# Optimization experiments

Hardware: AMD Instinct MI355X
Metric: run time of the kernel (lower is better)

Reference implementation:

```python
import jax, jax.numpy as jnp
import numpy as np
import math

HQ, HKV, DH, WIN = 16, 4, 128, 512
RMS_EPS = 1.1920929e-07  # torch F.rms_norm default eps = fp32 machine eps


def _apply_rope(x, cos, sin):
    # x: [B,H,T,Dh]; interleaved-pair rotation as in the torch code
    x_even = x[..., ::2]
    x_odd = x[..., 1::2]
    x_rot = jnp.stack((-x_odd, x_even), axis=-1).reshape(x.shape)
    return x * cos + x_rot * sin


def _rms_norm(x):
    return x * jax.lax.rsqrt(jnp.mean(x * x, axis=-1, keepdims=True) + RMS_EPS)


def setup_inputs() -> dict:
    key = jax.random.key(0)
    k1, k2, k3 = jax.random.split(key, 3)
    B, T, C = 2, 2048, 2048
    x = jax.random.normal(k1, (B, T, C), dtype=jnp.float32)
    w_qkv = jax.random.normal(k2, ((HQ + 2 * HKV) * DH, C), dtype=jnp.float32) * 0.02
    w_proj = jax.random.normal(k3, (C, C), dtype=jnp.float32) * 0.02
    return {"x": x, "w_qkv": w_qkv, "w_proj": w_proj}


def reference(x, w_qkv, w_proj):
    B, T, C = x.shape
    rep = HQ // HKV
    qkv = x @ w_qkv.T  # [B,T,(Hq+2Hkv)*Dh]
    q, k, v = jnp.split(qkv, [HQ * DH, (HQ + HKV) * DH], axis=-1)
    Q = q.reshape(B, T, HQ, DH).transpose(0, 2, 1, 3)   # [B,Hq,T,Dh]
    K = k.reshape(B, T, HKV, DH).transpose(0, 2, 1, 3)  # [B,Hkv,T,Dh]
    V = v.reshape(B, T, HKV, DH).transpose(0, 2, 1, 3)
    # GQA expansion (repeat_interleave on head dim)
    K = jnp.repeat(K, rep, axis=1)
    V = jnp.repeat(V, rep, axis=1)
    # RoPE tables: freqs [T, Dh/2] -> cos/sin [1,1,T,Dh] via repeat_interleave(2)
    inv_freq = 1.0 / (10000.0 ** (jnp.arange(0, DH, 2, dtype=jnp.float32) / DH))
    freqs = jnp.arange(T, dtype=jnp.float32)[:, None] * inv_freq[None, :]
    cos = jnp.repeat(jnp.cos(freqs), 2, axis=-1)[None, None]
    sin = jnp.repeat(jnp.sin(freqs), 2, axis=-1)[None, None]
    Q = _rms_norm(_apply_rope(Q, cos, sin))
    K = _rms_norm(_apply_rope(K, cos, sin))
    scores = jnp.einsum('bhqd,bhkd->bhqk', Q, K) / math.sqrt(DH)
    i = jnp.arange(T)[:, None]
    j = jnp.arange(T)[None, :]
    mask = (i >= j) & ((i - j) < WIN)  # causal sliding window
    scores = jnp.where(mask[None, None], scores, -jnp.inf)
    attn = jax.nn.softmax(scores, axis=-1)
    y = jnp.einsum('bhqk,bhkd->bhqd', attn, V)
    y = y.transpose(0, 2, 1, 3).reshape(B, T, C)
    return y @ w_proj.T
```

## Files before the change

### kernel.cpp

```cpp
#include <hip/hip_runtime.h>
#include <stdint.h>

#define T_SEQ 2048
#define NB    2
#define DHD   128
#define NHQ   16
#define NHKV  4
#define SWIN  512
#define CDIM  2048
#define QKVN  3072
#define GBK   32

typedef __attribute__((ext_vector_type(8))) short short8;
typedef __attribute__((ext_vector_type(4))) float f32x4;
typedef __attribute__((ext_vector_type(16))) float f32x16;
typedef __attribute__((ext_vector_type(4))) unsigned int u32x4;
typedef __attribute__((address_space(3))) unsigned int lds_u32;
typedef __attribute__((address_space(1))) const unsigned int gbl_u32;

__device__ __forceinline__ unsigned short f2bf(float f) {
  unsigned int u = __float_as_uint(f);
  u += 0x7fffu + ((u >> 16) & 1u);
  return (unsigned short)(u >> 16);
}
__device__ __forceinline__ float bf2f(unsigned int h) {
  return __uint_as_float(h << 16);
}
__device__ __forceinline__ float exp2_fast(float x) {
  float r;
  asm("v_exp_f32 %0, %1" : "=v"(r) : "v"(x));
  return r;
}

__global__ __launch_bounds__(256) void k_f2bf3(const float* __restrict__ a, unsigned short* __restrict__ oa, int na4,
                                               const float* __restrict__ b, unsigned short* __restrict__ ob, int nb4,
                                               const float* __restrict__ c, unsigned short* __restrict__ oc, int nc4) {
  const int n = na4 + nb4 + nc4;
  for (int i = blockIdx.x * 256 + threadIdx.x; i < n; i += gridDim.x * 256) {
    const float* src; unsigned short* dst; int j = i;
    if (j < na4) { src = a; dst = oa; }
    else if (j < na4 + nb4) { j -= na4; src = b; dst = ob; }
    else { j -= na4 + nb4; src = c; dst = oc; }
    float4 v = reinterpret_cast<const float4*>(src)[j];
    uint2 o;
    o.x = ((unsigned int)f2bf(v.y) << 16) | f2bf(v.x);
    o.y = ((unsigned int)f2bf(v.w) << 16) | f2bf(v.z);
    reinterpret_cast<uint2*>(dst)[j] = o;
  }
}

__global__ __launch_bounds__(256) void k_trig(float* __restrict__ tbl) {
  int i = blockIdx.x * 256 + threadIdx.x;
  if (i >= T_SEQ * 64) return;
  int t = i >> 6, f = i & 63;
  float invf = powf(10000.f, -(float)f * (1.f / 64.f));
  float ang = (float)t * invf;
  tbl[i] = cosf(ang);
  tbl[T_SEQ * 64 + i] = sinf(ang);
}

template<int OUT_BF16>
__global__ __launch_bounds__(512) void k_gemm128(const unsigned short* __restrict__ A,
                                                 const unsigned short* __restrict__ B,
                                                 void* __restrict__ Cout,
                                                 int M, int N, int K, int nbx) {
  extern __shared__ __align__(16) char lds[];
  const int tid = threadIdx.x, lane = tid & 63, wid = tid >> 6;
  const int lr = lane & 15, lg = lane >> 4;
  const int wr = wid >> 2, wcn = wid & 3;

  const int nwg = gridDim.x, cpx = nwg >> 3;
  const int id = (int)blockIdx.x;
  const int sid = (id & 7) * cpx + (id >> 3);
  const int by = sid / nbx, bx = sid - by * nbx;

  const unsigned short* Ab = A + (size_t)by * 128 * K;
  const unsigned short* Bb = B + (size_t)bx * 256 * K;

  const int row0 = tid >> 2;
  const int blk  = tid & 3;
  const int col0 = ((blk * 16) ^ (((row0 >> 1) & 3) << 4)) >> 1;
  const unsigned short* pA0 = Ab + (size_t)row0 * K + col0;
  const unsigned short* pB0 = Bb + (size_t)row0 * K + col0;
  const unsigned short* pB1 = pB0 + (size_t)128 * K;

  const int sw  = ((lg ^ ((lr >> 1) & 3)) << 4);
  const int arb = (wr * 64 + lr) * 64 + sw;
  const int brb = (wcn * 64 + lr) * 64 + sw;

  f32x4 acc[4][4];
#pragma unroll
  for (int mi = 0; mi < 4; ++mi)
#pragma unroll
    for (int ni = 0; ni < 4; ++ni)
#pragma unroll
      for (int r = 0; r < 4; ++r) acc[mi][ni][r] = 0.f;

#define STAGE(t, sl_) do {                                                             \
    const int ko_ = (t) * GBK;                                                         \
    __builtin_amdgcn_global_load_lds((gbl_u32*)(pA0 + ko_),                            \
        (lds_u32*)(lds + (sl_) * 24576 + wid * 1024), 16, 0, 0);                       \
    __builtin_amdgcn_global_load_lds((gbl_u32*)(pB0 + ko_),                            \
        (lds_u32*)(lds + (sl_) * 24576 + 8192 + wid * 1024), 16, 0, 0);                \
    __builtin_amdgcn_global_load_lds((gbl_u32*)(pB1 + ko_),                            \
        (lds_u32*)(lds + (sl_) * 24576 + 16384 + wid * 1024), 16, 0, 0);               \
  } while (0)

#define COMPUTE(sl_) do {                                                              \
    const char* As_ = lds + (sl_) * 24576;                                             \
    const char* Bs_ = As_ + 8192;                                                      \
    short8 afr[4], bfr[4];                                                             \
    _Pragma("unroll") for (int mi = 0; mi < 4; ++mi)                                   \
      afr[mi] = *reinterpret_cast<const short8*>(As_ + arb + mi * 1024);               \
    _Pragma("unroll") for (int ni = 0; ni < 4; ++ni)                                   \
      bfr[ni] = *reinterpret_cast<const short8*>(Bs_ + brb + ni * 1024);               \
    __builtin_amdgcn_s_setprio(1);                                                     \
    _Pragma("unroll") for (int mi = 0; mi < 4; ++mi)                                   \
      _Pragma("unroll") for (int ni = 0; ni < 4; ++ni)                                 \
        acc[mi][ni] = __builtin_amdgcn_mfma_f32_16x16x32_bf16(afr[mi], bfr[ni],        \
                                                              acc[mi][ni], 0, 0, 0);   \
    __builtin_amdgcn_s_setprio(0);                                                     \
  } while (0)

#define WAITBAR(n) do {                                                                \
    asm volatile("s_waitcnt vmcnt(" #n ")" ::: "memory");                              \
    __builtin_amdgcn_s_barrier();                                                      \
    asm volatile("" ::: "memory");                                                     \
  } while (0)

  const int nt = K / GBK;
  STAGE(0, 0); STAGE(1, 1);
  int sc = 0, ss = 2;
  for (int t = 0; t < nt - 2; ++t) {
    WAITBAR(3);
    STAGE(t + 2, ss);
    COMPUTE(sc);
    sc = (sc == 2) ? 0 : sc + 1;
    ss = (ss == 2) ? 0 : ss + 1;
  }
  WAITBAR(3);
  COMPUTE(sc);
  sc = (sc == 2) ? 0 : sc + 1;
  WAITBAR(0);
  COMPUTE(sc);

#undef STAGE
#undef COMPUTE
#undef WAITBAR

#pragma unroll
  for (int mi = 0; mi < 4; ++mi) {
    const int row0c = by * 128 + wr * 64 + mi * 16 + lg * 4;
#pragma unroll
    for (int ni = 0; ni < 4; ++ni) {
      const int col = bx * 256 + wcn * 64 + ni * 16 + lr;
#pragma unroll
      for (int r = 0; r < 4; ++r) {
        size_t idx = (size_t)(row0c + r) * N + col;
        if (OUT_BF16) ((unsigned short*)Cout)[idx] = f2bf(acc[mi][ni][r]);
        else          ((float*)Cout)[idx] = acc[mi][ni][r];
      }
    }
  }
}

__global__ __launch_bounds__(256) void k_rope_rms(const unsigned short* __restrict__ qkv,
                                                  const float* __restrict__ tbl,
                                                  unsigned short* __restrict__ Qo,
                                                  unsigned short* __restrict__ Ko) {
  const int lane = threadIdx.x & 63, wid = threadIdx.x >> 6;
  const int job = blockIdx.x * 4 + wid;
  const int row = job / 20;
  const int hh  = job - row * 20;
  const int b = row >> 11, t = row & (T_SEQ - 1);
  const unsigned short* src;
  unsigned short* dst;
  float scale;
  if (hh < NHQ) {
    src = qkv + (size_t)row * QKVN + hh * DHD;
    dst = Qo + (((size_t)b * NHQ + hh) * T_SEQ + t) * DHD;
    scale = 0.1275173019f;
  } else {
    int h = hh - NHQ;
    src = qkv + (size_t)row * QKVN + CDIM + h * DHD;
    dst = Ko + (((size_t)b * NHKV + h) * T_SEQ + t) * DHD;
    scale = 1.f;
  }
  unsigned int pr = *reinterpret_cast<const unsigned int*>(src + lane * 2);
  float xe = bf2f(pr & 0xffffu), xo = bf2f(pr >> 16);
  float c = tbl[t * 64 + lane], s = tbl[T_SEQ * 64 + t * 64 + lane];
  float e = xe * c - xo * s;
  float o = xo * c + xe * s;
  float ss = e * e + o * o;
#pragma unroll
  for (int off = 1; off < 64; off <<= 1) ss += __shfl_xor(ss, off);
  float rn = rsqrtf(ss * (1.f / 128.f) + 1.1920929e-07f) * scale;
  unsigned short eb = f2bf(e * rn), ob = f2bf(o * rn);
  *reinterpret_cast<unsigned int*>(dst + lane * 2) = ((unsigned int)ob << 16) | eb;
}

__global__ __launch_bounds__(256) void k_vtrans(const unsigned short* __restrict__ qkv,
                                                unsigned short* __restrict__ Vt) {
  __shared__ unsigned short tile[64][65];
  const int blk = blockIdx.x;
  const int dt = blk & 1;
  const int tt = (blk >> 1) & 31;
  const int h = (blk >> 6) & 3;
  const int b = blk >> 8;
  const int t0 = tt * 64, d0 = dt * 64;
#pragma unroll
  for (int i = 0; i < 16; ++i) {
    int idx = i * 256 + threadIdx.x;
    int tl = idx >> 6, dl = idx & 63;
    tile[tl][dl] = qkv[(size_t)(b * T_SEQ + t0 + tl) * QKVN + (CDIM + NHKV * DHD) + h * DHD + d0 + dl];
  }
  __syncthreads();
#pragma unroll
  for (int i = 0; i < 16; ++i) {
    int idx = i * 256 + threadIdx.x;
    int dl = idx >> 6, tl = idx & 63;
    Vt[((size_t)(b * NHKV + h) * DHD + d0 + dl) * T_SEQ + t0 + tl] = tile[tl][dl];
  }
}

__global__ __launch_bounds__(256) void k_attn(const unsigned short* __restrict__ Q,
                                              const unsigned short* __restrict__ K,
                                              const unsigned short* __restrict__ Vt,
                                              unsigned short* __restrict__ Y) {
  __shared__ __align__(16) char lds[49152];
  const int tid = threadIdx.x, lane = tid & 63, wid = tid >> 6;
  const int l31 = lane & 31, hi = lane >> 5;

  const int id = (int)blockIdx.x;
  const int sid = (id & 7) * 64 + (id >> 3);
  const int qt = sid & 15;
  const int h = (sid >> 4) & 15;
  const int b = sid >> 8;
  const int hkv = h >> 2;
  const int q0 = qt * 128;
  const int q0g = q0 + wid * 32;

  const unsigned short* Qp = Q + (((size_t)b * NHQ + h) * T_SEQ + q0g) * DHD;
  const char* Kbyte = (const char*)(K + ((size_t)b * NHKV + hkv) * T_SEQ * DHD);
  const char* Vbyte = (const char*)(Vt + ((size_t)b * NHKV + hkv) * DHD * T_SEQ);

  const int ksrc0 = (tid >> 4) * 256 + (((tid & 15) * 16) ^ (((tid >> 4) & 7) << 4));
  const int vsrc0 = (tid >> 2) * 4096 + (((tid & 3) * 16) ^ (((tid >> 2) & 3) << 4));

  const int ksw = (l31 & 7) << 4;
  const int vsw = (l31 & 3) << 4;

#define STAGEKV(k0_, sb_) do {                                                           \
    const char* kt_ = Kbyte + (size_t)(k0_) * 256;                                       \
    const char* vt_ = Vbyte + (size_t)(k0_) * 2;                                         \
    __builtin_amdgcn_global_load_lds((gbl_u32*)(kt_ + ksrc0),                            \
        (lds_u32*)(lds + (sb_) + wid * 1024), 16, 0, 0);                                 \
    __builtin_amdgcn_global_load_lds((gbl_u32*)(kt_ + ksrc0 + 4096),                     \
        (lds_u32*)(lds + (sb_) + 4096 + wid * 1024), 16, 0, 0);                          \
    __builtin_amdgcn_global_load_lds((gbl_u32*)(vt_ + vsrc0),                            \
        (lds_u32*)(lds + (sb_) + 8192 + wid * 1024), 16, 0, 0);                          \
    __builtin_amdgcn_global_load_lds((gbl_u32*)(vt_ + vsrc0 + 262144),                   \
        (lds_u32*)(lds + (sb_) + 12288 + wid * 1024), 16, 0, 0);                         \
  } while (0)

  const int kt0 = (q0 >= SWIN) ? ((q0 - (SWIN - 1)) >> 5) : 0;
  const int kth = (q0 + 127) >> 5;

  STAGEKV(kt0 * 32, 0);

  short8 qf[8];
#pragma unroll
  for (int ds = 0; ds < 8; ++ds)
    qf[ds] = *reinterpret_cast<const short8*>(Qp + (size_t)l31 * DHD + ds * 16 + hi * 8);

  f32x16 accO[4];
#pragma unroll
  for (int dt = 0; dt < 4; ++dt)
#pragma unroll
    for (int r = 0; r < 16; ++r) accO[dt][r] = 0.f;
  float m = -1e30f, l = 0.f;
  const int qg = q0g + l31;

  int sl = 0;
  for (int t = kt0; t <= kth; ++t) {
    const int sln = (sl == 2) ? 0 : sl + 1;
    if (t < kth) {
      STAGEKV((t + 1) * 32, sln * 16384);
      asm volatile("s_waitcnt vmcnt(4)" ::: "memory");
    } else {
      asm volatile("s_waitcnt vmcnt(0)" ::: "memory");
    }
    __builtin_amdgcn_s_barrier();

    const int k0 = t * 32;
    if (k0 <= q0g && k0 + 31 >= q0g - (SWIN - 1)) {
      const char* kbase = lds + sl * 16384;
      const char* vbase = kbase + 8192;

      short8 kf[8];
#pragma unroll
      for (int ds = 0; ds < 8; ++ds)
        kf[ds] = *reinterpret_cast<const short8*>(kbase + l31 * 256 + ((ds * 32 + hi * 16) ^ ksw));

      f32x16 s;
#pragma unroll
      for (int r = 0; r < 16; ++r) s[r] = 0.f;
      __builtin_amdgcn_s_setprio(1);
#pragma unroll
      for (int ds = 0; ds < 8; ++ds)
        s = __builtin_amdgcn_mfma_f32_32x32x16_bf16(kf[ds], qf[ds], s, 0, 0, 0);
      __builtin_amdgcn_s_setprio(0);

      if (k0 < q0g - 480 || k0 >= q0g) {
#pragma unroll
        for (int r = 0; r < 16; ++r) {
          int kk = k0 + (r & 3) + 8 * (r >> 2) + 4 * hi;
          if (kk > qg || qg - kk >= SWIN) s[r] = -1e30f;
        }
      }

      float mx[8];
#pragma unroll
      for (int j = 0; j < 8; ++j) mx[j] = fmaxf(s[2 * j], s[2 * j + 1]);
      float a0 = fmaxf(mx[0], mx[1]), a1 = fmaxf(mx[2], mx[3]);
      float a2 = fmaxf(mx[4], mx[5]), a3 = fmaxf(mx[6], mx[7]);
      float tmax = fmaxf(fmaxf(a0, a1), fmaxf(a2, a3));
      tmax = fmaxf(tmax, __shfl_xor(tmax, 32));

      float mn = m;
      if (!__all(tmax <= m + 8.f)) {
        mn = fmaxf(m, tmax);
        float alpha = exp2_fast(m - mn);
        l *= alpha;
#pragma unroll
        for (int dt = 0; dt < 4; ++dt)
#pragma unroll
          for (int r = 0; r < 16; ++r) accO[dt][r] *= alpha;
        m = mn;
      }

#pragma unroll
      for (int r = 0; r < 16; ++r) s[r] = exp2_fast(s[r] - mn);
      float sx[8];
#pragma unroll
      for (int j = 0; j < 8; ++j) sx[j] = s[2 * j] + s[2 * j + 1];
      float b0 = sx[0] + sx[1], b1 = sx[2] + sx[3], b2 = sx[4] + sx[5], b3 = sx[6] + sx[7];
      float ps = (b0 + b1) + (b2 + b3);
      ps += __shfl_xor(ps, 32);
      l += ps;

      unsigned int w[8];
#pragma unroll
      for (int j = 0; j < 8; ++j)
        asm("v_cvt_pk_bf16_f32 %0, %1, %2" : "=v"(w[j]) : "v"(s[2 * j]), "v"(s[2 * j + 1]));
      asm("v_permlane32_swap_b32 %0, %1" : "+v"(w[0]), "+v"(w[2]));
      asm("v_permlane32_swap_b32 %0, %1" : "+v"(w[1]), "+v"(w[3]));
      asm("v_permlane32_swap_b32 %0, %1" : "+v"(w[4]), "+v"(w[6]));
      asm("v_permlane32_swap_b32 %0, %1" : "+v"(w[5]), "+v"(w[7]));
      u32x4 p0 = {w[0], w[1], w[2], w[3]};
      u32x4 p1 = {w[4], w[5], w[6], w[7]};
      short8 pf0 = __builtin_bit_cast(short8, p0);
      short8 pf1 = __builtin_bit_cast(short8, p1);

      __builtin_amdgcn_s_setprio(1);
#pragma unroll
      for (int dt = 0; dt < 4; ++dt) {
        const char* vrow = vbase + (dt * 2048 + l31 * 64);
        short8 vf0 = *reinterpret_cast<const short8*>(vrow + ((hi * 16) ^ vsw));
        short8 vf1 = *reinterpret_cast<const short8*>(vrow + ((32 + hi * 16) ^ vsw));
        accO[dt] = __builtin_amdgcn_mfma_f32_32x32x16_bf16(vf0, pf0, accO[dt], 0, 0, 0);
        accO[dt] = __builtin_amdgcn_mfma_f32_32x32x16_bf16(vf1, pf1, accO[dt], 0, 0, 0);
      }
      __builtin_amdgcn_s_setprio(0);
    }
    sl = sln;
  }
#undef STAGEKV

  __syncthreads();

  float inv = 1.f / l;
  char* obc = lds + wid * 8192;
#pragma unroll
  for (int dt = 0; dt < 4; ++dt)
#pragma unroll
    for (int j = 0; j < 8; ++j) {
      float a = accO[dt][2 * j] * inv, c = accO[dt][2 * j + 1] * inv;
      unsigned int wv;
      asm("v_cvt_pk_bf16_f32 %0, %1, %2" : "=v"(wv) : "v"(a), "v"(c));
      int d = dt * 32 + 2 * (j & 1) + 8 * (j >> 1) + 4 * hi;
      *reinterpret_cast<unsigned int*>(obc + l31 * 256 + ((d * 2) ^ ksw)) = wv;
    }
#pragma unroll
  for (int i = 0; i < 8; ++i) {
    int chunk = i * 64 + lane;
    int row = chunk >> 4, c8 = chunk & 15;
    short8 v = *reinterpret_cast<const short8*>(obc + row * 256 + ((c8 * 16) ^ ((row & 7) << 4)));
    *reinterpret_cast<short8*>(Y + ((size_t)b * T_SEQ + q0g + row) * CDIM + h * DHD + c8 * 8) = v;
  }
}

extern "C" void kernel_launch(void* const* d_in, const int* in_sizes, int n_in,
                              void* d_out, int out_size, void* d_ws, size_t ws_size,
                              hipStream_t stream) {
  const float* x     = (const float*)d_in[0];
  const float* wqkv  = (const float*)d_in[1];
  const float* wproj = (const float*)d_in[2];
  float* out = (float*)d_out;

  char* ws = (char*)d_ws;
  unsigned short* xb     = (unsigned short*)(ws + 0);
  unsigned short* wqkvb  = (unsigned short*)(ws + 16777216);
  unsigned short* wprojb = (unsigned short*)(ws + 29360128);
  unsigned short* qkvb   = (unsigned short*)(ws + 37748736);
  unsigned short* Qb     = (unsigned short*)(ws + 62914560);
  unsigned short* Kb     = (unsigned short*)(ws + 79691776);
  unsigned short* Vtb    = (unsigned short*)(ws + 83886080);
  float* tbl             = (float*)(ws + 88080384);
  unsigned short* yb     = xb;

  k_f2bf3<<<2048, 256, 0, stream>>>(x, xb, (NB * T_SEQ * CDIM) / 4,
                                    wqkv, wqkvb, (QKVN * CDIM) / 4,
                                    wproj, wprojb, (CDIM * CDIM) / 4);
  k_trig<<<(T_SEQ * 64 + 255) / 256, 256, 0, stream>>>(tbl);

  k_gemm128<1><<<(NB * T_SEQ / 128) * (QKVN / 256), 512, 73728, stream>>>(
      xb, wqkvb, qkvb, NB * T_SEQ, QKVN, CDIM, QKVN / 256);
  k_rope_rms<<<(NB * T_SEQ * (NHQ + NHKV)) / 4, 256, 0, stream>>>(qkvb, tbl, Qb, Kb);
  k_vtrans<<<NB * NHKV * 32 * 2, 256, 0, stream>>>(qkvb, Vtb);
  k_attn<<<NB * NHQ * (T_SEQ / 128), 256, 0, stream>>>(Qb, Kb, Vtb, yb);
  k_gemm128<0><<<(NB * T_SEQ / 128) * (CDIM / 256), 512, 73728, stream>>>(
      yb, wprojb, out, NB * T_SEQ, CDIM, CDIM, CDIM / 256);
}
```

Before: 179.5 us.

## Use 256x256 GEMM tiles with 64-wide K steps and phased double buffering

After: 215.8 us. 1.2x slower.

```diff
diff --git a/kernel.cpp b/kernel.cpp
--- a/kernel.cpp
+++ b/kernel.cpp
@@ -9,7 +9,6 @@
 #define SWIN  512
 #define CDIM  2048
 #define QKVN  3072
-#define GBK   32
 
 typedef __attribute__((ext_vector_type(8))) short short8;
 typedef __attribute__((ext_vector_type(4))) float f32x4;
@@ -60,10 +59,10 @@
 }
 
 template<int OUT_BF16>
-__global__ __launch_bounds__(512) void k_gemm128(const unsigned short* __restrict__ A,
-                                                 const unsigned short* __restrict__ B,
-                                                 void* __restrict__ Cout,
-                                                 int M, int N, int K, int nbx) {
+__global__ __launch_bounds__(512) void k_gemm8p(const unsigned short* __restrict__ A,
+                                                const unsigned short* __restrict__ B,
+                                                void* __restrict__ Cout,
+                                                int M, int N, int K, int nbx) {
   extern __shared__ __align__(16) char lds[];
   const int tid = threadIdx.x, lane = tid & 63, wid = tid >> 6;
   const int lr = lane & 15, lg = lane >> 4;
@@ -74,83 +73,87 @@
   const int sid = (id & 7) * cpx + (id >> 3);
   const int by = sid / nbx, bx = sid - by * nbx;
 
-  const unsigned short* Ab = A + (size_t)by * 128 * K;
-  const unsigned short* Bb = B + (size_t)bx * 256 * K;
-
-  const int row0 = tid >> 2;
-  const int blk  = tid & 3;
-  const int col0 = ((blk * 16) ^ (((row0 >> 1) & 3) << 4)) >> 1;
-  const unsigned short* pA0 = Ab + (size_t)row0 * K + col0;
-  const unsigned short* pB0 = Bb + (size_t)row0 * K + col0;
-  const unsigned short* pB1 = pB0 + (size_t)128 * K;
-
-  const int sw  = ((lg ^ ((lr >> 1) & 3)) << 4);
-  const int arb = (wr * 64 + lr) * 64 + sw;
-  const int brb = (wcn * 64 + lr) * 64 + sw;
-
-  f32x4 acc[4][4];
-#pragma unroll
-  for (int mi = 0; mi < 4; ++mi)
+  const char* Ab = (const char*)(A + (size_t)by * 256 * K);
+  const char* Bb = (const char*)(B + (size_t)bx * 256 * K);
+
+  const int colb = ((tid & 7) * 16) ^ (((tid >> 4) & 7) << 4);
+  const char* pAb = Ab + (size_t)(tid >> 3) * K * 2 + colb;
+  const char* pBb = Bb + (size_t)(tid >> 3) * K * 2 + colb;
+  const size_t rowstep = (size_t)64 * K * 2;
+
+  const int rsw = (lr >> 1) << 4;
+  const int aoff0 = (wr * 128 + lr) * 128;
+  const int boff0 = 32768 + (wcn * 64 + lr) * 128;
+  const int csel0 = (lg * 16) ^ rsw;
+  const int csel1 = (64 + lg * 16) ^ rsw;
+
+  f32x4 acc[8][4];
+#pragma unroll
+  for (int mi = 0; mi < 8; ++mi)
 #pragma unroll
     for (int ni = 0; ni < 4; ++ni)
 #pragma unroll
       for (int r = 0; r < 4; ++r) acc[mi][ni][r] = 0.f;
 
-#define STAGE(t, sl_) do {                                                             \
-    const int ko_ = (t) * GBK;                                                         \
-    __builtin_amdgcn_global_load_lds((gbl_u32*)(pA0 + ko_),                            \
-        (lds_u32*)(lds + (sl_) * 24576 + wid * 1024), 16, 0, 0);                       \
-    __builtin_amdgcn_global_load_lds((gbl_u32*)(pB0 + ko_),                            \
-        (lds_u32*)(lds + (sl_) * 24576 + 8192 + wid * 1024), 16, 0, 0);                \
-    __builtin_amdgcn_global_load_lds((gbl_u32*)(pB1 + ko_),                            \
-        (lds_u32*)(lds + (sl_) * 24576 + 16384 + wid * 1024), 16, 0, 0);               \
+#define STAGE(t_, sl_) do {                                                            \
+    const char* at_ = pAb + (size_t)(t_) * 128;                                        \
+    const char* bt_ = pBb + (size_t)(t_) * 128;                                        \
+    _Pragma("unroll") for (int j = 0; j < 4; ++j) {                                    \
+      __builtin_amdgcn_global_load_lds((gbl_u32*)(at_ + (size_t)j * rowstep),          \
+          (lds_u32*)(lds + (sl_) * 65536 + j * 8192 + wid * 1024), 16, 0, 0);          \
+      __builtin_amdgcn_global_load_lds((gbl_u32*)(bt_ + (size_t)j * rowstep),          \
+          (lds_u32*)(lds + (sl_) * 65536 + 32768 + j * 8192 + wid * 1024), 16, 0, 0);  \
+    }                                                                                  \
   } while (0)
 
-#define COMPUTE(sl_) do {                                                              \
-    const char* As_ = lds + (sl_) * 24576;                                             \
-    const char* Bs_ = As_ + 8192;                                                      \
-    short8 afr[4], bfr[4];                                                             \
-    _Pragma("unroll") for (int mi = 0; mi < 4; ++mi)                                   \
-      afr[mi] = *reinterpret_cast<const short8*>(As_ + arb + mi * 1024);               \
-    _Pragma("unroll") for (int ni = 0; ni < 4; ++ni)                                   \
-      bfr[ni] = *reinterpret_cast<const short8*>(Bs_ + brb + ni * 1024);               \
+#define PHASE(q_) do {                                                                 \
+    short8 paf[4][2], pbf[2][2];                                                       \
+    _Pragma("unroll") for (int m2 = 0; m2 < 4; ++m2) {                                 \
+      paf[m2][0] = *(const short8*)(sbp + aoff0 + (((q_) & 1) * 4 + m2) * 2048 + csel0); \
+      paf[m2][1] = *(const short8*)(sbp + aoff0 + (((q_) & 1) * 4 + m2) * 2048 + csel1); \
+    }                                                                                  \
+    _Pragma("unroll") for (int n2 = 0; n2 < 2; ++n2) {                                 \
+      pbf[n2][0] = *(const short8*)(sbp + boff0 + (((q_) >> 1) * 2 + n2) * 2048 + csel0); \
+      pbf[n2][1] = *(const short8*)(sbp + boff0 + (((q_) >> 1) * 2 + n2) * 2048 + csel1); \
+    }                                                                                  \
     __builtin_amdgcn_s_setprio(1);                                                     \
-    _Pragma("unroll") for (int mi = 0; mi < 4; ++mi)                                   \
-      _Pragma("unroll") for (int ni = 0; ni < 4; ++ni)                                 \
-        acc[mi][ni] = __builtin_amdgcn_mfma_f32_16x16x32_bf16(afr[mi], bfr[ni],        \
-                                                              acc[mi][ni], 0, 0, 0);   \
+    _Pragma("unroll") for (int m2 = 0; m2 < 4; ++m2)                                   \
+      _Pragma("unroll") for (int n2 = 0; n2 < 2; ++n2) {                               \
+        f32x4 acv = acc[((q_) & 1) * 4 + m2][((q_) >> 1) * 2 + n2];                    \
+        acv = __builtin_amdgcn_mfma_f32_16x16x32_bf16(paf[m2][0], pbf[n2][0], acv, 0, 0, 0); \
+        acv = __builtin_amdgcn_mfma_f32_16x16x32_bf16(paf[m2][1], pbf[n2][1], acv, 0, 0, 0); \
+        acc[((q_) & 1) * 4 + m2][((q_) >> 1) * 2 + n2] = acv;                          \
+      }                                                                                \
     __builtin_amdgcn_s_setprio(0);                                                     \
+    __builtin_amdgcn_s_barrier();                                                      \
   } while (0)
 
-#define WAITBAR(n) do {                                                                \
-    asm volatile("s_waitcnt vmcnt(" #n ")" ::: "memory");                              \
-    __builtin_amdgcn_s_barrier();                                                      \
-    asm volatile("" ::: "memory");                                                     \
-  } while (0)
-
-  const int nt = K / GBK;
-  STAGE(0, 0); STAGE(1, 1);
-  int sc = 0, ss = 2;
-  for (int t = 0; t < nt - 2; ++t) {
-    WAITBAR(3);
-    STAGE(t + 2, ss);
-    COMPUTE(sc);
-    sc = (sc == 2) ? 0 : sc + 1;
-    ss = (ss == 2) ? 0 : ss + 1;
-  }
-  WAITBAR(3);
-  COMPUTE(sc);
-  sc = (sc == 2) ? 0 : sc + 1;
-  WAITBAR(0);
-  COMPUTE(sc);
+  const int nt = K >> 6;
+  STAGE(0, 0);
+  STAGE(1, 1);
+  asm volatile("s_waitcnt vmcnt(8)" ::: "memory");
+  __builtin_amdgcn_s_barrier();
+
+  for (int t = 0; t < nt; ++t) {
+    const int s = t & 1;
+    const char* sbp = lds + s * 65536;
+    PHASE(0); PHASE(1); PHASE(2); PHASE(3);
+    if (t + 2 < nt) {
+      STAGE(t + 2, s);
+      asm volatile("s_waitcnt vmcnt(8)" ::: "memory");
+      __builtin_amdgcn_s_barrier();
+    } else if (t + 1 < nt) {
+      asm volatile("s_waitcnt vmcnt(0)" ::: "memory");
+      __builtin_amdgcn_s_barrier();
+    }
+  }
 
 #undef STAGE
-#undef COMPUTE
-#undef WAITBAR
-
-#pragma unroll
-  for (int mi = 0; mi < 4; ++mi) {
-    const int row0c = by * 128 + wr * 64 + mi * 16 + lg * 4;
+#undef PHASE
+
+#pragma unroll
+  for (int mi = 0; mi < 8; ++mi) {
+    const int row0c = by * 256 + wr * 128 + mi * 16 + lg * 4;
 #pragma unroll
     for (int ni = 0; ni < 4; ++ni) {
       const int col = bx * 256 + wcn * 64 + ni * 16 + lr;
@@ -424,11 +427,11 @@
                                     wproj, wprojb, (CDIM * CDIM) / 4);
   k_trig<<<(T_SEQ * 64 + 255) / 256, 256, 0, stream>>>(tbl);
 
-  k_gemm128<1><<<(NB * T_SEQ / 128) * (QKVN / 256), 512, 73728, stream>>>(
+  k_gemm8p<1><<<(NB * T_SEQ / 256) * (QKVN / 256), 512, 131072, stream>>>(
       xb, wqkvb, qkvb, NB * T_SEQ, QKVN, CDIM, QKVN / 256);
   k_rope_rms<<<(NB * T_SEQ * (NHQ + NHKV)) / 4, 256, 0, stream>>>(qkvb, tbl, Qb, Kb);
   k_vtrans<<<NB * NHKV * 32 * 2, 256, 0, stream>>>(qkvb, Vtb);
   k_attn<<<NB * NHQ * (T_SEQ / 128), 256, 0, stream>>>(Qb, Kb, Vtb, yb);
-  k_gemm128<0><<<(NB * T_SEQ / 128) * (CDIM / 256), 512, 73728, stream>>>(
+  k_gemm8p<0><<<(NB * T_SEQ / 256) * (CDIM / 256), 512, 131072, stream>>>(
       yb, wprojb, out, NB * T_SEQ, CDIM, CDIM, CDIM / 256);
 }
```

## Add 256x192-tile QKV GEMM so the grid fills one wave

Applied to the files above, without the earlier changes.

After: 169.6 us. 1.06x faster.

```diff
diff --git a/kernel.cpp b/kernel.cpp
--- a/kernel.cpp
+++ b/kernel.cpp
@@ -57,6 +57,129 @@
   float ang = (float)t * invf;
   tbl[i] = cosf(ang);
   tbl[T_SEQ * 64 + i] = sinf(ang);
+}
+
+template<int OUT_BF16>
+__global__ __launch_bounds__(512, 2) void k_gemm192(const unsigned short* __restrict__ A,
+                                                    const unsigned short* __restrict__ B,
+                                                    void* __restrict__ Cout,
+                                                    int M, int N, int K, int nbx) {
+  extern __shared__ __align__(16) char lds[];
+  const int tid = threadIdx.x, lane = tid & 63, wid = tid >> 6;
+  const int lr = lane & 15, lg = lane >> 4;
+  const int wr = wid >> 2, wcn = wid & 3;
+
+  const int nwg = gridDim.x, cpx = nwg >> 3;
+  const int id = (int)blockIdx.x;
+  const int sid = (id & 7) * cpx + (id >> 3);
+  const int by = sid / nbx, bx = sid - by * nbx;
+
+  const unsigned short* Ab = A + (size_t)by * 256 * K;
+  const unsigned short* Bb = B + (size_t)bx * 192 * K;
+
+  const int row0 = tid >> 2;
+  const int blk  = tid & 3;
+  const int col0 = ((blk * 16) ^ (((row0 >> 1) & 3) << 4)) >> 1;
+  const unsigned short* pA0 = Ab + (size_t)row0 * K + col0;
+  const unsigned short* pA1 = pA0 + (size_t)128 * K;
+  const unsigned short* pB0 = Bb + (size_t)row0 * K + col0;
+  const unsigned short* pB2 = pB0 + (size_t)128 * K;
+
+  const int sw  = ((lg ^ ((lr >> 1) & 3)) << 4);
+  const int arb = (wr * 128 + lr) * 64 + sw;
+  const int brb = 16384 + (wcn * 48 + lr) * 64 + sw;
+
+  f32x4 acc[8][3];
+#pragma unroll
+  for (int mi = 0; mi < 8; ++mi)
+#pragma unroll
+    for (int ni = 0; ni < 3; ++ni)
+#pragma unroll
+      for (int r = 0; r < 4; ++r) acc[mi][ni][r] = 0.f;
+
+#define STAGE(t) do {                                                                  \
+    const int sl_ = (t) & 3; const int ko_ = (t) * GBK;                                \
+    char* sb_ = lds + sl_ * 28672;                                                     \
+    __builtin_amdgcn_global_load_lds((gbl_u32*)(pA0 + ko_),                            \
+        (lds_u32*)(sb_ + wid * 1024), 16, 0, 0);                                       \
+    __builtin_amdgcn_global_load_lds((gbl_u32*)(pA1 + ko_),                            \
+        (lds_u32*)(sb_ + 8192 + wid * 1024), 16, 0, 0);                                \
+    __builtin_amdgcn_global_load_lds((gbl_u32*)(pB0 + ko_),                            \
+        (lds_u32*)(sb_ + 16384 + wid * 1024), 16, 0, 0);                               \
+    if (wid < 4)                                                                       \
+      __builtin_amdgcn_global_load_lds((gbl_u32*)(pB2 + ko_),                          \
+          (lds_u32*)(sb_ + 24576 + wid * 1024), 16, 0, 0);                             \
+    __builtin_amdgcn_global_load_lds((gbl_u32*)(pA1 + ko_),         \
+        (lds_u32*)(sb_ + 8192 + wid * 1024), 0, 0, 0);                                 \
+  } while (0)
+
+#undef STAGE
+#define STAGE(t) do {                                                                  \
+    const int sl_ = (t) & 3; const int ko_ = (t) * GBK;                                \
+    char* sb_ = lds + sl_ * 28672;                                                     \
+    __builtin_amdgcn_global_load_lds((gbl_u32*)(pA0 + ko_),                            \
+        (lds_u32*)(sb_ + wid * 1024), 16, 0, 0);                                       \
+    __builtin_amdgcn_global_load_lds((gbl_u32*)(pA1 + ko_),                            \
+        (lds_u32*)(sb_ + 8192 + wid * 1024), 16, 0, 0);                                \
+    __builtin_amdgcn_global_load_lds((gbl_u32*)(pB0 + ko_),                            \
+        (lds_u32*)(sb_ + 16384 + wid * 1024), 16, 0, 0);                               \
+    if (wid < 4)                                                                       \
+      __builtin_amdgcn_global_load_lds((gbl_u32*)(pB2 + ko_),                          \
+          (lds_u32*)(sb_ + 24576 + wid * 1024), 16, 0, 0);                             \
+  } while (0)
+
+#define COMPUTE(t) do {                                                                \
+    const int sl_ = (t) & 3;                                                           \
+    const char* sb_ = lds + sl_ * 28672;                                               \
+    short8 afr[8], bfr[3];                                                             \
+    _Pragma("unroll") for (int mi = 0; mi < 8; ++mi)                                   \
+      afr[mi] = *reinterpret_cast<const short8*>(sb_ + arb + mi * 1024);               \
+    _Pragma("unroll") for (int ni = 0; ni < 3; ++ni)                                   \
+      bfr[ni] = *reinterpret_cast<const short8*>(sb_ + brb + ni * 1024);               \
+    __builtin_amdgcn_s_setprio(1);                                                     \
+    _Pragma("unroll") for (int mi = 0; mi < 8; ++mi)                                   \
+      _Pragma("unroll") for (int ni = 0; ni < 3; ++ni)                                 \
+        acc[mi][ni] = __builtin_amdgcn_mfma_f32_16x16x32_bf16(afr[mi], bfr[ni],        \
+                                                              acc[mi][ni], 0, 0, 0);   \
+    __builtin_amdgcn_s_setprio(0);                                                     \
+  } while (0)
+
+#define WAITBAR2(nlo, nhi) do {                                                        \
+    if (wid < 4) asm volatile("s_waitcnt vmcnt(" #nlo ")" ::: "memory");               \
+    else         asm volatile("s_waitcnt vmcnt(" #nhi ")" ::: "memory");               \
+    __builtin_amdgcn_s_barrier();                                                      \
+    asm volatile("" ::: "memory");                                                     \
+  } while (0)
+
+  const int nt = K / GBK;
+  STAGE(0); STAGE(1); STAGE(2);
+  for (int t = 0; t < nt - 3; ++t) {
+    WAITBAR2(10, 8);
+    STAGE(t + 3);
+    COMPUTE(t);
+  }
+  WAITBAR2(10, 8); COMPUTE(nt - 3);
+  WAITBAR2(5, 4);  COMPUTE(nt - 2);
+  WAITBAR2(0, 0);  COMPUTE(nt - 1);
+
+#undef STAGE
+#undef COMPUTE
+#undef WAITBAR2
+
+#pragma unroll
+  for (int mi = 0; mi < 8; ++mi) {
+    const int row0c = by * 256 + wr * 128 + mi * 16 + lg * 4;
+#pragma unroll
+    for (int ni = 0; ni < 3; ++ni) {
+      const int col = bx * 192 + wcn * 48 + ni * 16 + lr;
+#pragma unroll
+      for (int r = 0; r < 4; ++r) {
+        size_t idx = (size_t)(row0c + r) * N + col;
+        if (OUT_BF16) ((unsigned short*)Cout)[idx] = f2bf(acc[mi][ni][r]);
+        else          ((float*)Cout)[idx] = acc[mi][ni][r];
+      }
+    }
+  }
 }
 
 template<int OUT_BF16>
@@ -424,11 +547,11 @@
                                     wproj, wprojb, (CDIM * CDIM) / 4);
   k_trig<<<(T_SEQ * 64 + 255) / 256, 256, 0, stream>>>(tbl);
 
-  k_gemm128<1><<<(NB * T_SEQ / 128) * (QKVN / 256), 512, 73728, stream>>>(
-      xb, wqkvb, qkvb, NB * T_SEQ, QKVN, CDIM, QKVN / 256);
+  k_gemm192<1><<<256, 512, 114688, stream>>>(
+      xb, wqkvb, qkvb, NB * T_SEQ, QKVN, CDIM, QKVN / 192);
   k_rope_rms<<<(NB * T_SEQ * (NHQ + NHKV)) / 4, 256, 0, stream>>>(qkvb, tbl, Qb, Kb);
   k_vtrans<<<NB * NHKV * 32 * 2, 256, 0, stream>>>(qkvb, Vtb);
   k_attn<<<NB * NHQ * (T_SEQ / 128), 256, 0, stream>>>(Qb, Kb, Vtb, yb);
-  k_gemm128<0><<<(NB * T_SEQ / 128) * (CDIM / 256), 512, 73728, stream>>>(
+  k_gemm128<0><<<256, 512, 73728, stream>>>(
       yb, wprojb, out, NB * T_SEQ, CDIM, CDIM, CDIM / 256);
 }
```
